# Optimization experiments

Hardware: AMD Instinct MI355X
Metric: run time of the kernel (lower is better)

The kernel has to match this reference:

```python
import jax, jax.numpy as jnp
import numpy as np

B, F, ND, NE = 1024, 1024, 256, 256

def setup_inputs() -> dict:
    key = jax.random.key(0)
    k1, k2, k3 = jax.random.split(key, 3)
    x = jax.random.normal(k1, (B, F), dtype=jnp.float32)
    # xavier-uniform-like init scale for (F+1, units)
    lim_d = float(np.sqrt(6.0 / (F + 1 + ND)))
    lim_e = float(np.sqrt(6.0 / (F + 1 + NE)))
    dilations = jax.random.uniform(k2, (F + 1, ND), minval=-lim_d, maxval=lim_d, dtype=jnp.float32)
    erosions = jax.random.uniform(k3, (F + 1, NE), minval=-lim_e, maxval=lim_e, dtype=jnp.float32)
    return {"x": x, "dilations": dilations, "erosions": erosions}

def reference(x, dilations, erosions):
    b = x.shape[0]
    # append a zero 'bias' feature -> (b, F+1)
    xb = jnp.concatenate([x, jnp.zeros((b, 1), dtype=x.dtype)], axis=1)
    # tropical matmuls: max-plus (dilation), min-minus (erosion)
    dilated = jnp.max(xb[:, :, None] + dilations[None, :, :], axis=1)   # (b, ND)
    eroded = jnp.min(xb[:, :, None] - erosions[None, :, :], axis=1)     # (b, NE)
    return jnp.concatenate([eroded, dilated], axis=1)
```

## Files before the change

### kernel.cpp

```cpp
#include <hip/hip_runtime.h>
#include <math.h>

#define BB   1024
#define FF   1024
#define NOUT 512
#define NW   256
#define BT   128
#define CT   128
#define KT   64
#define KS   (FF / KT)

__global__ __launch_bounds__(256, 2) void trop_main(
    const float* __restrict__ x,
    const float* __restrict__ dil,
    const float* __restrict__ ero,
    float* __restrict__ ws)
{
    const int bx = blockIdx.x;
    const int by = blockIdx.y;
    const int bz = blockIdx.z;
    const bool is_ero = (bx < 2);
    const float* __restrict__ w = is_ero ? ero : dil;
    const int c0w = (bx & 1) * CT;
    const int r0 = by * BT;
    const float sgn = is_ero ? -1.0f : 1.0f;
    const int fb = bz * KT;

    __shared__ float lds_x[KT][BT];
    __shared__ float lds_w[KT][CT];

    const int tid = threadIdx.x;
    const int cg = tid & 15;
    const int rg = tid >> 4;

#pragma unroll
    for (int it = 0; it < 8; ++it) {
        const int idx = it * 256 + tid;
        const int r = idx >> 4;
        const int g = idx & 15;
        const float4 v = *(const float4*)(x + (size_t)(r0 + r) * FF + fb + g * 4);
        const int rb = r >> 3, rl = r & 7;
        const float vv[4] = {v.x, v.y, v.z, v.w};
#pragma unroll
        for (int q = 0; q < 4; ++q) {
            const int f = g * 4 + q;
            lds_x[f][((rb ^ (f & 15)) << 3) | rl] = sgn * vv[q];
        }
    }
#pragma unroll
    for (int it = 0; it < 8; ++it) {
        const int idx = it * 256 + tid;
        const int f = idx >> 5;
        const int c4 = idx & 31;
        *(float4*)&lds_w[f][c4 * 4] =
            *(const float4*)(w + (size_t)(fb + f) * NW + c0w + c4 * 4);
    }
    __syncthreads();

    float acc[8][8];
#pragma unroll
    for (int i = 0; i < 8; ++i)
#pragma unroll
        for (int j = 0; j < 8; ++j) acc[i][j] = -INFINITY;

#pragma unroll 2
    for (int ff = 0; ff < KT; ff += 2) {
        const int s0 = ((rg ^ (ff & 15)) << 3);
        const int s1 = ((rg ^ ((ff + 1) & 15)) << 3);
        const float4 xa0 = *(const float4*)&lds_x[ff][s0];
        const float4 xb0 = *(const float4*)&lds_x[ff][s0 + 4];
        const float4 xa1 = *(const float4*)&lds_x[ff + 1][s1];
        const float4 xb1 = *(const float4*)&lds_x[ff + 1][s1 + 4];
        const float4 wa0 = *(const float4*)&lds_w[ff][cg * 4];
        const float4 wb0 = *(const float4*)&lds_w[ff][64 + cg * 4];
        const float4 wa1 = *(const float4*)&lds_w[ff + 1][cg * 4];
        const float4 wb1 = *(const float4*)&lds_w[ff + 1][64 + cg * 4];
        const float xr0[8] = {xa0.x, xa0.y, xa0.z, xa0.w, xb0.x, xb0.y, xb0.z, xb0.w};
        const float xr1[8] = {xa1.x, xa1.y, xa1.z, xa1.w, xb1.x, xb1.y, xb1.z, xb1.w};
        const float wc0[8] = {wa0.x, wa0.y, wa0.z, wa0.w, wb0.x, wb0.y, wb0.z, wb0.w};
        const float wc1[8] = {wa1.x, wa1.y, wa1.z, wa1.w, wb1.x, wb1.y, wb1.z, wb1.w};
#pragma unroll
        for (int i = 0; i < 8; ++i)
#pragma unroll
            for (int j = 0; j < 8; ++j) {
                acc[i][j] = fmaxf(acc[i][j],
                                  fmaxf(xr0[i] + wc0[j], xr1[i] + wc1[j]));
            }
    }

    if (bz == KS - 1) {
        const float4 ba = *(const float4*)(w + (size_t)FF * NW + c0w + cg * 4);
        const float4 bb = *(const float4*)(w + (size_t)FF * NW + c0w + 64 + cg * 4);
        const float bc[8] = {ba.x, ba.y, ba.z, ba.w, bb.x, bb.y, bb.z, bb.w};
#pragma unroll
        for (int i = 0; i < 8; ++i)
#pragma unroll
            for (int j = 0; j < 8; ++j) acc[i][j] = fmaxf(acc[i][j], bc[j]);
    }

    float* plane = ws + (size_t)bz * (BB * NOUT);
    const int cglob = bx * CT + cg * 4;
#pragma unroll
    for (int i = 0; i < 8; ++i) {
        const int row = r0 + rg * 8 + i;
        float4 v0, v1;
        v0.x = sgn * acc[i][0]; v0.y = sgn * acc[i][1];
        v0.z = sgn * acc[i][2]; v0.w = sgn * acc[i][3];
        v1.x = sgn * acc[i][4]; v1.y = sgn * acc[i][5];
        v1.z = sgn * acc[i][6]; v1.w = sgn * acc[i][7];
        *(float4*)(plane + (size_t)row * NOUT + cglob) = v0;
        *(float4*)(plane + (size_t)row * NOUT + cglob + 64) = v1;
    }
}

__global__ __launch_bounds__(256) void trop_combine(
    const float* __restrict__ ws, float* __restrict__ out)
{
    const int i4 = blockIdx.x * 256 + threadIdx.x;
    const bool ero = (i4 & 127) < 64;
    const int stride4 = BB * NOUT / 4;
    float4 v = ((const float4*)ws)[i4];
#pragma unroll
    for (int z = 1; z < KS; ++z) {
        const float4 u = ((const float4*)ws)[(size_t)z * stride4 + i4];
        if (ero) {
            v.x = fminf(v.x, u.x); v.y = fminf(v.y, u.y);
            v.z = fminf(v.z, u.z); v.w = fminf(v.w, u.w);
        } else {
            v.x = fmaxf(v.x, u.x); v.y = fmaxf(v.y, u.y);
            v.z = fmaxf(v.z, u.z); v.w = fmaxf(v.w, u.w);
        }
    }
    ((float4*)out)[i4] = v;
}

extern "C" void kernel_launch(void* const* d_in, const int* in_sizes, int n_in,
                              void* d_out, int out_size, void* d_ws, size_t ws_size,
                              hipStream_t stream) {
    const float* x = (const float*)d_in[0];
    const float* dil = (const float*)d_in[1];
    const float* ero = (const float*)d_in[2];
    float* out = (float*)d_out;
    float* ws = (float*)d_ws;

    dim3 grid(4, BB / BT, KS);
    trop_main<<<grid, 256, 0, stream>>>(x, dil, ero, ws);
    trop_combine<<<BB * NOUT / 4 / 256, 256, 0, stream>>>(ws, out);
}
```

Baseline: 92.35 us.

## Pre-transpose x and read operands directly from global memory instead of LDS

Adds a transpose kernel that writes x as feature-major into workspace, then the main kernel drops its LDS staging and reads x and weights straight from global memory (cache) inside the loop. Erosion is computed as max of (w - x) and negated in the combine pass, which removes the sign multiplies in the main kernel. This removes LDS writes, the swizzle and the barrier, but adds an extra kernel launch and global traffic, and relies on cache hits for operand reuse across threads.

```diff
diff --git a/kernel.cpp b/kernel.cpp
--- a/kernel.cpp
+++ b/kernel.cpp
@@ -7,11 +7,38 @@
 #define NW   256
 #define BT   128
 #define CT   128
-#define KT   64
-#define KS   (FF / KT)
+#define KS   16
+#define KT   (FF / KS)
+#define XT_OFF ((size_t)KS * BB * NOUT)
+
+__global__ __launch_bounds__(256) void trop_transpose(
+    const float* __restrict__ x, float* __restrict__ xt)
+{
+    __shared__ float t[64][65];
+    const int f0 = blockIdx.x * 64;
+    const int r0 = blockIdx.y * 64;
+    const int tr = threadIdx.x >> 4;
+    const int tc = threadIdx.x & 15;
+#pragma unroll
+    for (int q = 0; q < 4; ++q) {
+        const int r = tr + q * 16;
+        const float4 v = *(const float4*)(x + (size_t)(r0 + r) * FF + f0 + tc * 4);
+        t[r][tc * 4 + 0] = v.x; t[r][tc * 4 + 1] = v.y;
+        t[r][tc * 4 + 2] = v.z; t[r][tc * 4 + 3] = v.w;
+    }
+    __syncthreads();
+#pragma unroll
+    for (int q = 0; q < 4; ++q) {
+        const int f = tr + q * 16;
+        float4 v;
+        v.x = t[tc * 4 + 0][f]; v.y = t[tc * 4 + 1][f];
+        v.z = t[tc * 4 + 2][f]; v.w = t[tc * 4 + 3][f];
+        *(float4*)(xt + (size_t)(f0 + f) * BB + r0 + tc * 4) = v;
+    }
+}
 
 __global__ __launch_bounds__(256, 2) void trop_main(
-    const float* __restrict__ x,
+    const float* __restrict__ xt,
     const float* __restrict__ dil,
     const float* __restrict__ ero,
     float* __restrict__ ws)
@@ -23,39 +50,10 @@
     const float* __restrict__ w = is_ero ? ero : dil;
     const int c0w = (bx & 1) * CT;
     const int r0 = by * BT;
-    const float sgn = is_ero ? -1.0f : 1.0f;
-    const int fb = bz * KT;
-
-    __shared__ float lds_x[KT][BT];
-    __shared__ float lds_w[KT][CT];
 
     const int tid = threadIdx.x;
     const int cg = tid & 15;
     const int rg = tid >> 4;
-
-#pragma unroll
-    for (int it = 0; it < 8; ++it) {
-        const int idx = it * 256 + tid;
-        const int r = idx >> 4;
-        const int g = idx & 15;
-        const float4 v = *(const float4*)(x + (size_t)(r0 + r) * FF + fb + g * 4);
-        const int rb = r >> 3, rl = r & 7;
-        const float vv[4] = {v.x, v.y, v.z, v.w};
-#pragma unroll
-        for (int q = 0; q < 4; ++q) {
-            const int f = g * 4 + q;
-            lds_x[f][((rb ^ (f & 15)) << 3) | rl] = sgn * vv[q];
-        }
-    }
-#pragma unroll
-    for (int it = 0; it < 8; ++it) {
-        const int idx = it * 256 + tid;
-        const int f = idx >> 5;
-        const int c4 = idx & 31;
-        *(float4*)&lds_w[f][c4 * 4] =
-            *(const float4*)(w + (size_t)(fb + f) * NW + c0w + c4 * 4);
-    }
-    __syncthreads();
 
     float acc[8][8];
 #pragma unroll
@@ -63,29 +61,55 @@
 #pragma unroll
         for (int j = 0; j < 8; ++j) acc[i][j] = -INFINITY;
 
+    const float* xp = xt + (size_t)(bz * KT) * BB + r0 + rg * 8;
+    const float* wp = w + (size_t)(bz * KT) * NW + c0w + cg * 4;
+
+    if (is_ero) {
 #pragma unroll 2
-    for (int ff = 0; ff < KT; ff += 2) {
-        const int s0 = ((rg ^ (ff & 15)) << 3);
-        const int s1 = ((rg ^ ((ff + 1) & 15)) << 3);
-        const float4 xa0 = *(const float4*)&lds_x[ff][s0];
-        const float4 xb0 = *(const float4*)&lds_x[ff][s0 + 4];
-        const float4 xa1 = *(const float4*)&lds_x[ff + 1][s1];
-        const float4 xb1 = *(const float4*)&lds_x[ff + 1][s1 + 4];
-        const float4 wa0 = *(const float4*)&lds_w[ff][cg * 4];
-        const float4 wb0 = *(const float4*)&lds_w[ff][64 + cg * 4];
-        const float4 wa1 = *(const float4*)&lds_w[ff + 1][cg * 4];
-        const float4 wb1 = *(const float4*)&lds_w[ff + 1][64 + cg * 4];
-        const float xr0[8] = {xa0.x, xa0.y, xa0.z, xa0.w, xb0.x, xb0.y, xb0.z, xb0.w};
-        const float xr1[8] = {xa1.x, xa1.y, xa1.z, xa1.w, xb1.x, xb1.y, xb1.z, xb1.w};
-        const float wc0[8] = {wa0.x, wa0.y, wa0.z, wa0.w, wb0.x, wb0.y, wb0.z, wb0.w};
-        const float wc1[8] = {wa1.x, wa1.y, wa1.z, wa1.w, wb1.x, wb1.y, wb1.z, wb1.w};
+        for (int ff = 0; ff < KT; ff += 2) {
+            const float4 xa0 = *(const float4*)(xp);
+            const float4 xb0 = *(const float4*)(xp + 4);
+            const float4 xa1 = *(const float4*)(xp + BB);
+            const float4 xb1 = *(const float4*)(xp + BB + 4);
+            const float4 wa0 = *(const float4*)(wp);
+            const float4 wb0 = *(const float4*)(wp + 64);
+            const float4 wa1 = *(const float4*)(wp + NW);
+            const float4 wb1 = *(const float4*)(wp + NW + 64);
+            xp += 2 * BB; wp += 2 * NW;
+            const float xr0[8] = {xa0.x, xa0.y, xa0.z, xa0.w, xb0.x, xb0.y, xb0.z, xb0.w};
+            const float xr1[8] = {xa1.x, xa1.y, xa1.z, xa1.w, xb1.x, xb1.y, xb1.z, xb1.w};
+            const float wc0[8] = {wa0.x, wa0.y, wa0.z, wa0.w, wb0.x, wb0.y, wb0.z, wb0.w};
+            const float wc1[8] = {wa1.x, wa1.y, wa1.z, wa1.w, wb1.x, wb1.y, wb1.z, wb1.w};
 #pragma unroll
-        for (int i = 0; i < 8; ++i)
+            for (int i = 0; i < 8; ++i)
 #pragma unroll
-            for (int j = 0; j < 8; ++j) {
-                acc[i][j] = fmaxf(acc[i][j],
-                                  fmaxf(xr0[i] + wc0[j], xr1[i] + wc1[j]));
-            }
+                for (int j = 0; j < 8; ++j)
+                    acc[i][j] = fmaxf(acc[i][j],
+                                      fmaxf(wc0[j] - xr0[i], wc1[j] - xr1[i]));
+        }
+    } else {
+#pragma unroll 2
+        for (int ff = 0; ff < KT; ff += 2) {
+            const float4 xa0 = *(const float4*)(xp);
+            const float4 xb0 = *(const float4*)(xp + 4);
+            const float4 xa1 = *(const float4*)(xp + BB);
+            const float4 xb1 = *(const float4*)(xp + BB + 4);
+            const float4 wa0 = *(const float4*)(wp);
+            const float4 wb0 = *(const float4*)(wp + 64);
+            const float4 wa1 = *(const float4*)(wp + NW);
+            const float4 wb1 = *(const float4*)(wp + NW + 64);
+            xp += 2 * BB; wp += 2 * NW;
+            const float xr0[8] = {xa0.x, xa0.y, xa0.z, xa0.w, xb0.x, xb0.y, xb0.z, xb0.w};
+            const float xr1[8] = {xa1.x, xa1.y, xa1.z, xa1.w, xb1.x, xb1.y, xb1.z, xb1.w};
+            const float wc0[8] = {wa0.x, wa0.y, wa0.z, wa0.w, wb0.x, wb0.y, wb0.z, wb0.w};
+            const float wc1[8] = {wa1.x, wa1.y, wa1.z, wa1.w, wb1.x, wb1.y, wb1.z, wb1.w};
+#pragma unroll
+            for (int i = 0; i < 8; ++i)
+#pragma unroll
+                for (int j = 0; j < 8; ++j)
+                    acc[i][j] = fmaxf(acc[i][j],
+                                      fmaxf(xr0[i] + wc0[j], xr1[i] + wc1[j]));
+        }
     }
 
     if (bz == KS - 1) {
@@ -104,10 +128,8 @@
     for (int i = 0; i < 8; ++i) {
         const int row = r0 + rg * 8 + i;
         float4 v0, v1;
-        v0.x = sgn * acc[i][0]; v0.y = sgn * acc[i][1];
-        v0.z = sgn * acc[i][2]; v0.w = sgn * acc[i][3];
-        v1.x = sgn * acc[i][4]; v1.y = sgn * acc[i][5];
-        v1.z = sgn * acc[i][6]; v1.w = sgn * acc[i][7];
+        v0.x = acc[i][0]; v0.y = acc[i][1]; v0.z = acc[i][2]; v0.w = acc[i][3];
+        v1.x = acc[i][4]; v1.y = acc[i][5]; v1.z = acc[i][6]; v1.w = acc[i][7];
         *(float4*)(plane + (size_t)row * NOUT + cglob) = v0;
         *(float4*)(plane + (size_t)row * NOUT + cglob + 64) = v1;
     }
@@ -117,20 +139,16 @@
     const float* __restrict__ ws, float* __restrict__ out)
 {
     const int i4 = blockIdx.x * 256 + threadIdx.x;
-    const bool ero = (i4 & 127) < 64;
+    const float sgn = ((i4 & 127) < 64) ? -1.0f : 1.0f;
     const int stride4 = BB * NOUT / 4;
     float4 v = ((const float4*)ws)[i4];
 #pragma unroll
     for (int z = 1; z < KS; ++z) {
         const float4 u = ((const float4*)ws)[(size_t)z * stride4 + i4];
-        if (ero) {
-            v.x = fminf(v.x, u.x); v.y = fminf(v.y, u.y);
-            v.z = fminf(v.z, u.z); v.w = fminf(v.w, u.w);
-        } else {
-            v.x = fmaxf(v.x, u.x); v.y = fmaxf(v.y, u.y);
-            v.z = fmaxf(v.z, u.z); v.w = fmaxf(v.w, u.w);
-        }
+        v.x = fmaxf(v.x, u.x); v.y = fmaxf(v.y, u.y);
+        v.z = fmaxf(v.z, u.z); v.w = fmaxf(v.w, u.w);
     }
+    v.x *= sgn; v.y *= sgn; v.z *= sgn; v.w *= sgn;
     ((float4*)out)[i4] = v;
 }
 
@@ -142,8 +160,13 @@
     const float* ero = (const float*)d_in[2];
     float* out = (float*)d_out;
     float* ws = (float*)d_ws;
+    float* xt = ws + XT_OFF;
+
+    dim3 tgrid(FF / 64, BB / 64);
+    trop_transpose<<<tgrid, 256, 0, stream>>>(x, xt);
 
     dim3 grid(4, BB / BT, KS);
-    trop_main<<<grid, 256, 0, stream>>>(x, dil, ero, ws);
+    trop_main<<<grid, 256, 0, stream>>>(xt, dil, ero, ws);
+
     trop_combine<<<BB * NOUT / 4 / 256, 256, 0, stream>>>(ws, out);
 }
```

Result: slower. 96.99 us (+5.0%).
